# Optimization experiments

Hardware: AMD Instinct MI355X
Metric: run time of the kernel (lower is better)

The kernel has to match this reference:

```python
import jax, jax.numpy as jnp
import numpy as np

FREQ = 0.3  # oscillation_freq
EPS = 1e-12


def _spectral_normalize(W, u):
    # torch spectral_norm, training mode: one power iteration with no-grad u,v,
    # then sigma = u' @ W @ v with gradient flowing through W only.
    v = W.T @ u
    v = jax.lax.stop_gradient(v / (jnp.linalg.norm(v) + EPS))
    u2 = W @ v
    u2 = jax.lax.stop_gradient(u2 / (jnp.linalg.norm(u2) + EPS))
    sigma = u2 @ (W @ v)
    return W / sigma


def setup_inputs() -> dict:
    key = jax.random.key(0)
    ks = jax.random.split(key, 11)
    B, D_IN, H, D_OUT = 4096, 1024, 1024, 256

    def xavier(k, shape, gain=0.4):
        a = gain * np.sqrt(6.0 / (shape[0] + shape[1]))
        return jax.random.uniform(k, shape, minval=-a, maxval=a, dtype=jnp.float32)

    def bias(k, fan_in, n):
        b = 1.0 / np.sqrt(fan_in)
        return jax.random.uniform(k, (n,), minval=-b, maxval=b, dtype=jnp.float32)

    def unit(k, n):
        u = jax.random.normal(k, (n,), dtype=jnp.float32)
        return u / (jnp.linalg.norm(u) + EPS)

    return {
        "x": jax.random.normal(ks[0], (B, D_IN), dtype=jnp.float32),
        "W_in": xavier(ks[1], (H, D_IN)),
        "b_in": bias(ks[2], D_IN, H),
        "W_rec": xavier(ks[3], (H, H)),
        "b_rec": bias(ks[4], H, H),
        "W_out": xavier(ks[5], (D_OUT, H)),
        "b_out": bias(ks[6], H, D_OUT),
        "u_in": unit(ks[7], H),
        "u_rec": unit(ks[8], H),
        "u_out": unit(ks[9], D_OUT),
        "steps": 30,
    }


def reference(x, W_in, b_in, W_rec, b_rec, W_out, b_out, u_in, u_rec, u_out, steps):
    Wi = _spectral_normalize(W_in, u_in)
    Wr = _spectral_normalize(W_rec, u_rec)
    Wo = _spectral_normalize(W_out, u_out)

    x_proj = x @ Wi.T + b_in  # [B, H]
    h0 = jnp.zeros_like(x_proj)

    def step(h, t):
        modulation = 1.0 + 0.1 * jnp.sin(FREQ * t)
        h = jnp.tanh(x_proj + (h @ Wr.T + b_rec) * modulation)
        return h, None

    h, _ = jax.lax.scan(step, h0, jnp.arange(steps, dtype=jnp.float32))
    return h @ Wo.T + b_out
```

## Files before the change

kernel.cpp:

```cpp
#include <hip/hip_runtime.h>
#include <hip/hip_bf16.h>
#include <math.h>
#include <stdint.h>


#define EPSF 1e-12f

typedef short bf16x8 __attribute__((ext_vector_type(8)));
typedef float f32x4 __attribute__((ext_vector_type(4)));

struct Mods { float m[32]; };

__device__ __forceinline__ unsigned short f2bf(float f) {
  union { float f; unsigned u; } v; v.f = f;
  unsigned r = v.u + 0x7FFFu + ((v.u >> 16) & 1u);
  return (unsigned short)(r >> 16);
}

__device__ __forceinline__ unsigned cvt_pk_bf16(float lo, float hi) {
  unsigned r;
  asm("v_cvt_pk_bf16_f32 %0, %1, %2" : "=v"(r) : "v"(lo), "v"(hi));
  return r;
}

__device__ __forceinline__ float tanh_fast(float x) {
  float e = __expf(2.0f * x);
  float r = __builtin_amdgcn_rcpf(e + 1.0f);
  return fmaf(-2.0f, r, 1.0f);
}

__device__ __forceinline__ float block_reduce_sum(float x) {
#pragma unroll
  for (int o = 32; o > 0; o >>= 1) x += __shfl_down(x, o, 64);
  __shared__ float sm[8];
  int lane = threadIdx.x & 63, w = threadIdx.x >> 6;
  if (lane == 0) sm[w] = x;
  __syncthreads();
  float t = 0.f;
  if (threadIdx.x == 0) {
    int nw = (int)(blockDim.x >> 6);
    for (int i = 0; i < nw; ++i) t += sm[i];
  }
  return t;
}


__global__ void spec_col3(const float* __restrict__ Wi, const float* __restrict__ Wr,
                          const float* __restrict__ Wo, const float* __restrict__ ui,
                          const float* __restrict__ ur, const float* __restrict__ uo,
                          float* __restrict__ v) {
  int z = blockIdx.z;
  const float* W = (z == 0) ? Wi : (z == 1) ? Wr : Wo;
  const float* u = (z == 0) ? ui : (z == 1) ? ur : uo;
  int M = (z == 2) ? 256 : 1024;
  int i0 = blockIdx.y * 64;
  if (i0 >= M) return;
  int j = blockIdx.x * blockDim.x + threadIdx.x;
  float acc = 0.f;
  for (int i = i0; i < i0 + 64; ++i)
    acc += W[(size_t)i * 1024 + j] * u[i];
  atomicAdd(&v[z * 1024 + j], acc);
}

__global__ void reduce3(const float* __restrict__ Wi, const float* __restrict__ Wr,
                        const float* __restrict__ Wo, const float* __restrict__ v,
                        float* __restrict__ S) {
  int bid = blockIdx.x;
  if (bid >= 2304) {
    int z = bid - 2304;
    float acc = 0.f;
    for (int i = threadIdx.x; i < 1024; i += blockDim.x) {
      float x = v[z * 1024 + i];
      acc += x * x;
    }
    float t = block_reduce_sum(acc);
    if (threadIdx.x == 0) S[z] = t;
    return;
  }
  int z = (bid < 1024) ? 0 : (bid < 2048) ? 1 : 2;
  int row = bid - ((z == 0) ? 0 : (z == 1) ? 1024 : 2048);
  const float* W = (z == 0) ? Wi : (z == 1) ? Wr : Wo;
  const float* vv = v + z * 1024;
  float acc = 0.f;
  for (int j = threadIdx.x; j < 1024; j += blockDim.x)
    acc += W[(size_t)row * 1024 + j] * vv[j];
  float r = block_reduce_sum(acc);
  if (threadIdx.x == 0) atomicAdd(&S[3 + z], r * r);
}

__device__ __forceinline__ ushort4 cvt4e(float4 w, float s) {
  ushort4 r;
  r.x = f2bf(w.x * s); r.y = f2bf(w.y * s); r.z = f2bf(w.z * s); r.w = f2bf(w.w * s);
  return r;
}

__device__ __forceinline__ float inv_sigma(float nvsq, float wv2) {
  float nv = sqrtf(nvsq);
  float inv = 1.f / (nv + EPSF);
  float u2sq = wv2 * inv * inv;
  float nu = sqrtf(u2sq);
  float sigma = u2sq / (nu + EPSF);
  return 1.f / sigma;
}

__global__ void cvt_all(const float4* __restrict__ Wi, const float4* __restrict__ Wr,
                        const float4* __restrict__ Wo, const float4* __restrict__ x,
                        const float* __restrict__ S,
                        ushort4* __restrict__ oWi, ushort4* __restrict__ oWr,
                        ushort4* __restrict__ oWo, ushort4* __restrict__ ox) {
  float s6 = inv_sigma(S[0], S[3]);
  float s7 = inv_sigma(S[1], S[4]);
  float s8 = inv_sigma(S[2], S[5]);
  int stride = gridDim.x * blockDim.x;
  int t0 = blockIdx.x * blockDim.x + threadIdx.x;
  for (int i = t0; i < 262144; i += stride) {
    int n = i >> 8, ku = i & 255;
    int kc = ku >> 3, quad = (ku >> 1) & 3, j4 = ku & 1;
    oWi[(((n >> 4) * 32 + kc) * 64 + (n & 15) + 16 * quad) * 2 + j4] = cvt4e(Wi[i], s6);
  }
  for (int i = t0; i < 262144; i += stride) {
    int n = i >> 8, ku = i & 255;
    int kc = ku >> 3, quad = (ku >> 1) & 3, j4 = ku & 1;
    oWr[(((n >> 4) * 32 + kc) * 64 + (n & 15) + 16 * quad) * 2 + j4] = cvt4e(Wr[i], s7);
  }
  for (int i = t0; i < 65536; i += stride) {
    int n = i >> 8, ku = i & 255;
    int kc = ku >> 3, quad = (ku >> 1) & 3, j4 = ku & 1;
    oWo[(((n >> 4) * 32 + kc) * 64 + (n & 15) + 16 * quad) * 2 + j4] = cvt4e(Wo[i], s8);
  }
  for (int i = t0; i < 1048576; i += stride) {
    int m = i >> 8, ku = i & 255;
    int kc = ku >> 3, quad = (ku >> 1) & 3, j4 = ku & 1;
    ox[(size_t)(m >> 5) * 8192 +
       ((((m >> 4) & 1) * 32 + kc) * 64 + (m & 15) + 16 * quad) * 2 + j4] =
        cvt4e(x[i], 1.0f);
  }
}


template <int NF>
__device__ __forceinline__ void sweepT(const unsigned short* hsrc,
                                       const unsigned short* __restrict__ Wsrc,
                                       int lx, f32x4 acc[2][NF]) {
  bf16x8 hf[4][2], wf[4][NF];
#define LOADSET(S, KC)                                                      \
  {                                                                         \
    int kq = (KC) & 31;                                                     \
    hf[S][0] = *(const bf16x8*)(hsrc + kq * 512 + lx);                      \
    hf[S][1] = *(const bf16x8*)(hsrc + (32 + kq) * 512 + lx);               \
    _Pragma("unroll")                                                       \
    for (int nf = 0; nf < NF; ++nf)                                         \
      wf[S][nf] = *(const bf16x8*)(Wsrc + (nf * 32 + kq) * 512 + lx);       \
  }
  LOADSET(0, 0) LOADSET(1, 1) LOADSET(2, 2) LOADSET(3, 3)
#pragma unroll 1
  for (int kc = 0; kc < 32; kc += 4) {
#define STEP(S)                                                             \
    {                                                                       \
      __builtin_amdgcn_s_setprio(1);                                        \
      _Pragma("unroll")                                                     \
      for (int nf = 0; nf < NF; ++nf) {                                     \
        acc[0][nf] = __builtin_amdgcn_mfma_f32_16x16x32_bf16(               \
            wf[S][nf], hf[S][0], acc[0][nf], 0, 0, 0);                      \
        acc[1][nf] = __builtin_amdgcn_mfma_f32_16x16x32_bf16(               \
            wf[S][nf], hf[S][1], acc[1][nf], 0, 0, 0);                      \
      }                                                                     \
      __builtin_amdgcn_s_setprio(0);                                        \
      LOADSET(S, kc + S + 4)                                                \
    }
    STEP(0) STEP(1) STEP(2) STEP(3)
#undef STEP
  }
#undef LOADSET
}

__global__ __launch_bounds__(512, 1) void rnn_all(
    const unsigned short* __restrict__ xT,
    const unsigned short* __restrict__ WiT,
    const unsigned short* __restrict__ WrT,
    const unsigned short* __restrict__ WoT,
    const float* __restrict__ b_in,
    const float* __restrict__ b_rec,
    const float* __restrict__ b_out,
    float* __restrict__ outF,
    Mods mods) {
  __shared__ __align__(16) unsigned short hb[2 * 32768];

  const int tid = threadIdx.x;
  const int w = tid >> 6, lane = tid & 63;
  const int lrow = lane & 15, quad = lane >> 4;
  const int lx = lane * 8;
  const int m0 = (int)blockIdx.x * 32;
  const unsigned short* xb = xT + (size_t)blockIdx.x * 32768;

  f32x4 xpr[2][2][4];
#pragma unroll
  for (int nh = 0; nh < 2; ++nh) {
    f32x4 xa[2][4] = {};
    sweepT<4>(xb, WiT + (size_t)((w * 8 + nh * 4) * 32) * 512, lx, xa);
#pragma unroll
    for (int nf = 0; nf < 4; ++nf) {
      float4 bin4 = *(const float4*)&b_in[w * 128 + nh * 64 + nf * 16 + quad * 4];
#pragma unroll
      for (int mf = 0; mf < 2; ++mf) {
        xpr[nh][mf][nf][0] = xa[mf][nf][0] + bin4.x;
        xpr[nh][mf][nf][1] = xa[mf][nf][1] + bin4.y;
        xpr[nh][mf][nf][2] = xa[mf][nf][2] + bin4.z;
        xpr[nh][mf][nf][3] = xa[mf][nf][3] + bin4.w;
      }
    }
  }

  unsigned short* hcur = hb;
  unsigned short* hnxt = hb + 32768;
#pragma unroll 1
  for (int t = 0; t < 30; ++t) {
    const float mod = mods.m[t];
#pragma unroll
    for (int nh = 0; nh < 2; ++nh) {
      f32x4 acc[2][4] = {};
      if (t) sweepT<4>(hcur, WrT + (size_t)((w * 8 + nh * 4) * 32) * 512, lx, acc);
#pragma unroll
      for (int nf = 0; nf < 4; ++nf) {
        float4 br4 = *(const float4*)&b_rec[w * 128 + nh * 64 + nf * 16 + quad * 4];
        const int kcp = w * 4 + nh * 2 + (nf >> 1);
        const int lanep = lrow + 16 * ((nf * 2 + (quad >> 1)) & 3);
#pragma unroll
        for (int mf = 0; mf < 2; ++mf) {
          float h0 = tanh_fast(fmaf(acc[mf][nf][0] + br4.x, mod, xpr[nh][mf][nf][0]));
          float h1 = tanh_fast(fmaf(acc[mf][nf][1] + br4.y, mod, xpr[nh][mf][nf][1]));
          float h2 = tanh_fast(fmaf(acc[mf][nf][2] + br4.z, mod, xpr[nh][mf][nf][2]));
          float h3 = tanh_fast(fmaf(acc[mf][nf][3] + br4.w, mod, xpr[nh][mf][nf][3]));
          uint2 pk = {cvt_pk_bf16(h0, h1), cvt_pk_bf16(h2, h3)};
          *(uint2*)(hnxt + (mf * 32 + kcp) * 512 + lanep * 8 + (quad & 1) * 4) = pk;
        }
      }
    }
    __syncthreads();
    unsigned short* tmp = hcur; hcur = hnxt; hnxt = tmp;
  }

  {
    f32x4 ao[2][2] = {};
    sweepT<2>(hcur, WoT + (size_t)((w * 2) * 32) * 512, lx, ao);
#pragma unroll
    for (int nf = 0; nf < 2; ++nf) {
      float4 bo4 = *(const float4*)&b_out[w * 32 + nf * 16 + quad * 4];
#pragma unroll
      for (int mf = 0; mf < 2; ++mf) {
        float4 o;
        o.x = ao[mf][nf][0] + bo4.x;
        o.y = ao[mf][nf][1] + bo4.y;
        o.z = ao[mf][nf][2] + bo4.z;
        o.w = ao[mf][nf][3] + bo4.w;
        *(float4*)&outF[(size_t)(m0 + mf * 16 + lrow) * 256 + w * 32 + nf * 16 + quad * 4] = o;
      }
    }
  }
}

extern "C" void kernel_launch(void* const* d_in, const int* in_sizes, int n_in,
                              void* d_out, int out_size, void* d_ws, size_t ws_size,
                              hipStream_t stream) {
  const float* x     = (const float*)d_in[0];
  const float* W_in  = (const float*)d_in[1];
  const float* b_in  = (const float*)d_in[2];
  const float* W_rec = (const float*)d_in[3];
  const float* b_rec = (const float*)d_in[4];
  const float* W_out = (const float*)d_in[5];
  const float* b_out = (const float*)d_in[6];
  const float* u_in  = (const float*)d_in[7];
  const float* u_rec = (const float*)d_in[8];
  const float* u_out = (const float*)d_in[9];

  const int B = 4096, H = 1024;

  char* w = (char*)d_ws;
  float* S = (float*)w;
  float* v = S + 256;
  unsigned short* WiT = (unsigned short*)(w + 16384);
  unsigned short* WrT = WiT + (size_t)H * H;
  unsigned short* WoT = WrT + (size_t)H * H;
  unsigned short* xT  = WoT + (size_t)256 * H;

  hipMemsetAsync(w, 0, 16384, stream);

  dim3 t256(256);
  spec_col3<<<dim3(4, 16, 3), t256, 0, stream>>>(W_in, W_rec, W_out, u_in, u_rec, u_out, v);
  reduce3<<<2307, t256, 0, stream>>>(W_in, W_rec, W_out, v, S);
  cvt_all<<<1024, t256, 0, stream>>>((const float4*)W_in, (const float4*)W_rec,
                                     (const float4*)W_out, (const float4*)x, S,
                                     (ushort4*)WiT, (ushort4*)WrT,
                                     (ushort4*)WoT, (ushort4*)xT);

  Mods mods;
  for (int t = 0; t < 32; ++t) mods.m[t] = (float)(1.0 + 0.1 * sin(0.3 * (double)t));

  rnn_all<<<dim3(B / 32), dim3(512), 0, stream>>>(
      xT, WiT, WrT, WoT, b_in, b_rec, b_out, (float*)d_out, mods);
}
```

Baseline: 680.3 us.

## Split each batch tile across two cooperating blocks with global-memory flag sync

Each 32-row batch tile is now handled by two blocks, each owning half the hidden units. The 128-block grid becomes a 256-block cooperative launch, which uses more CUs on the GPU. The hidden state moves from LDS to a double-buffered global image, and partner blocks exchange a step counter through atomic flags. When both blocks sit on the same XCC, the acquire is replaced by a lighter cache invalidate. This adds a per-step cross-block spin wait and global-memory traffic for h, and relies on correct cache-coherence handling for correctness.

```diff
diff --git a/kernel.cpp b/kernel.cpp
--- a/kernel.cpp
+++ b/kernel.cpp
@@ -174,7 +174,7 @@
 #undef LOADSET
 }
 
-__global__ __launch_bounds__(512, 1) void rnn_all(
+__global__ __launch_bounds__(512, 2) void rnn_all(
     const unsigned short* __restrict__ xT,
     const unsigned short* __restrict__ WiT,
     const unsigned short* __restrict__ WrT,
@@ -182,79 +182,128 @@
     const float* __restrict__ b_in,
     const float* __restrict__ b_rec,
     const float* __restrict__ b_out,
+    unsigned short* __restrict__ himg,
+    unsigned* __restrict__ flags,
+    unsigned* __restrict__ xcds,
     float* __restrict__ outF,
     Mods mods) {
-  __shared__ __align__(16) unsigned short hb[2 * 32768];
-
   const int tid = threadIdx.x;
   const int w = tid >> 6, lane = tid & 63;
   const int lrow = lane & 15, quad = lane >> 4;
   const int lx = lane * 8;
-  const int m0 = (int)blockIdx.x * 32;
-  const unsigned short* xb = xT + (size_t)blockIdx.x * 32768;
-
-  f32x4 xpr[2][2][4];
-#pragma unroll
-  for (int nh = 0; nh < 2; ++nh) {
+  const int bid = (int)blockIdx.x;
+  const int p = bid & 127, s = bid >> 7;
+  const int m0 = p * 32;
+  const int nfbase = s * 32 + w * 4;
+  unsigned short* img0 = himg + (size_t)p * 65536;
+  unsigned short* img1 = img0 + 32768;
+  unsigned* myflag = flags + (size_t)(p * 2 + s) * 16;
+  unsigned* ptflag = flags + (size_t)(p * 2 + (1 - s)) * 16;
+  const unsigned short* xb = xT + (size_t)p * 32768;
+
+  unsigned myxcc = 0;
+  if (tid == 0) {
+    asm volatile("s_getreg_b32 %0, hwreg(HW_REG_XCC_ID)" : "=s"(myxcc));
+    __hip_atomic_store(xcds + (p * 2 + s), myxcc, __ATOMIC_RELEASE,
+                       __HIP_MEMORY_SCOPE_AGENT);
+  }
+
+  float4 brec4[4];
+#pragma unroll
+  for (int nf = 0; nf < 4; ++nf)
+    brec4[nf] = *(const float4*)&b_rec[s * 512 + w * 64 + nf * 16 + quad * 4];
+
+  f32x4 xpr[2][4];
+  {
     f32x4 xa[2][4] = {};
-    sweepT<4>(xb, WiT + (size_t)((w * 8 + nh * 4) * 32) * 512, lx, xa);
+    sweepT<4>(xb, WiT + (size_t)nfbase * 32 * 512, lx, xa);
 #pragma unroll
     for (int nf = 0; nf < 4; ++nf) {
-      float4 bin4 = *(const float4*)&b_in[w * 128 + nh * 64 + nf * 16 + quad * 4];
+      float4 bin4 = *(const float4*)&b_in[s * 512 + w * 64 + nf * 16 + quad * 4];
 #pragma unroll
       for (int mf = 0; mf < 2; ++mf) {
-        xpr[nh][mf][nf][0] = xa[mf][nf][0] + bin4.x;
-        xpr[nh][mf][nf][1] = xa[mf][nf][1] + bin4.y;
-        xpr[nh][mf][nf][2] = xa[mf][nf][2] + bin4.z;
-        xpr[nh][mf][nf][3] = xa[mf][nf][3] + bin4.w;
+        xpr[mf][nf][0] = xa[mf][nf][0] + bin4.x;
+        xpr[mf][nf][1] = xa[mf][nf][1] + bin4.y;
+        xpr[mf][nf][2] = xa[mf][nf][2] + bin4.z;
+        xpr[mf][nf][3] = xa[mf][nf][3] + bin4.w;
       }
     }
   }
 
-  unsigned short* hcur = hb;
-  unsigned short* hnxt = hb + 32768;
+  int fastv = 1;
+
 #pragma unroll 1
   for (int t = 0; t < 30; ++t) {
-    const float mod = mods.m[t];
-#pragma unroll
-    for (int nh = 0; nh < 2; ++nh) {
-      f32x4 acc[2][4] = {};
-      if (t) sweepT<4>(hcur, WrT + (size_t)((w * 8 + nh * 4) * 32) * 512, lx, acc);
-#pragma unroll
-      for (int nf = 0; nf < 4; ++nf) {
-        float4 br4 = *(const float4*)&b_rec[w * 128 + nh * 64 + nf * 16 + quad * 4];
-        const int kcp = w * 4 + nh * 2 + (nf >> 1);
-        const int lanep = lrow + 16 * ((nf * 2 + (quad >> 1)) & 3);
-#pragma unroll
-        for (int mf = 0; mf < 2; ++mf) {
-          float h0 = tanh_fast(fmaf(acc[mf][nf][0] + br4.x, mod, xpr[nh][mf][nf][0]));
-          float h1 = tanh_fast(fmaf(acc[mf][nf][1] + br4.y, mod, xpr[nh][mf][nf][1]));
-          float h2 = tanh_fast(fmaf(acc[mf][nf][2] + br4.z, mod, xpr[nh][mf][nf][2]));
-          float h3 = tanh_fast(fmaf(acc[mf][nf][3] + br4.w, mod, xpr[nh][mf][nf][3]));
-          uint2 pk = {cvt_pk_bf16(h0, h1), cvt_pk_bf16(h2, h3)};
-          *(uint2*)(hnxt + (mf * 32 + kcp) * 512 + lanep * 8 + (quad & 1) * 4) = pk;
+    f32x4 acc[2][4] = {};
+    if (t) {
+      if (tid == 0) {
+        while (__hip_atomic_load(ptflag, __ATOMIC_RELAXED,
+                                 __HIP_MEMORY_SCOPE_AGENT) < (unsigned)t)
+          __builtin_amdgcn_s_sleep(2);
+        if (t == 1) {
+          unsigned px = __hip_atomic_load(xcds + (p * 2 + (1 - s)),
+                                          __ATOMIC_RELAXED, __HIP_MEMORY_SCOPE_AGENT);
+          fastv = ((px & 15u) == (myxcc & 15u)) ? 1 : 0;
+        }
+        if (fastv) {
+          asm volatile("buffer_inv sc0" ::: "memory");
+        } else {
+          (void)__hip_atomic_load(ptflag, __ATOMIC_ACQUIRE, __HIP_MEMORY_SCOPE_AGENT);
         }
       }
+      __syncthreads();
+      sweepT<4>((t & 1) ? img0 : img1, WrT + (size_t)nfbase * 32 * 512, lx, acc);
+    }
+    const float mod = mods.m[t];
+    unsigned short* dst = (t & 1) ? img1 : img0;
+#pragma unroll
+    for (int nf = 0; nf < 4; ++nf) {
+      const int kcp = s * 16 + w * 2 + (nf >> 1);
+      const int lanep = lrow + 16 * (((nf & 1) * 2 + (quad >> 1)));
+#pragma unroll
+      for (int mf = 0; mf < 2; ++mf) {
+        float h0 = tanh_fast(fmaf(acc[mf][nf][0] + brec4[nf].x, mod, xpr[mf][nf][0]));
+        float h1 = tanh_fast(fmaf(acc[mf][nf][1] + brec4[nf].y, mod, xpr[mf][nf][1]));
+        float h2 = tanh_fast(fmaf(acc[mf][nf][2] + brec4[nf].z, mod, xpr[mf][nf][2]));
+        float h3 = tanh_fast(fmaf(acc[mf][nf][3] + brec4[nf].w, mod, xpr[mf][nf][3]));
+        uint2 pk = {cvt_pk_bf16(h0, h1), cvt_pk_bf16(h2, h3)};
+        *(uint2*)(dst + (mf * 32 + kcp) * 512 + lanep * 8 + (quad & 1) * 4) = pk;
+      }
     }
     __syncthreads();
-    unsigned short* tmp = hcur; hcur = hnxt; hnxt = tmp;
-  }
-
+    if (tid == 0) {
+      if (t == 0 || !fastv)
+        __hip_atomic_store(myflag, (unsigned)(t + 1), __ATOMIC_RELEASE,
+                           __HIP_MEMORY_SCOPE_AGENT);
+      else
+        __hip_atomic_store(myflag, (unsigned)(t + 1), __ATOMIC_RELAXED,
+                           __HIP_MEMORY_SCOPE_AGENT);
+    }
+  }
+
+  if (tid == 0) {
+    while (__hip_atomic_load(ptflag, __ATOMIC_RELAXED,
+                             __HIP_MEMORY_SCOPE_AGENT) < 30u)
+      __builtin_amdgcn_s_sleep(2);
+    if (fastv) {
+      asm volatile("buffer_inv sc0" ::: "memory");
+    } else {
+      (void)__hip_atomic_load(ptflag, __ATOMIC_ACQUIRE, __HIP_MEMORY_SCOPE_AGENT);
+    }
+  }
+  __syncthreads();
   {
-    f32x4 ao[2][2] = {};
-    sweepT<2>(hcur, WoT + (size_t)((w * 2) * 32) * 512, lx, ao);
-#pragma unroll
-    for (int nf = 0; nf < 2; ++nf) {
-      float4 bo4 = *(const float4*)&b_out[w * 32 + nf * 16 + quad * 4];
-#pragma unroll
-      for (int mf = 0; mf < 2; ++mf) {
-        float4 o;
-        o.x = ao[mf][nf][0] + bo4.x;
-        o.y = ao[mf][nf][1] + bo4.y;
-        o.z = ao[mf][nf][2] + bo4.z;
-        o.w = ao[mf][nf][3] + bo4.w;
-        *(float4*)&outF[(size_t)(m0 + mf * 16 + lrow) * 256 + w * 32 + nf * 16 + quad * 4] = o;
-      }
+    f32x4 ao[2][1] = {};
+    sweepT<1>(img1, WoT + (size_t)((s * 8 + w) * 32) * 512, lx, ao);
+    float4 bo4 = *(const float4*)&b_out[s * 128 + w * 16 + quad * 4];
+#pragma unroll
+    for (int mf = 0; mf < 2; ++mf) {
+      float4 o;
+      o.x = ao[mf][0][0] + bo4.x;
+      o.y = ao[mf][0][1] + bo4.y;
+      o.z = ao[mf][0][2] + bo4.z;
+      o.w = ao[mf][0][3] + bo4.w;
+      *(float4*)&outF[(size_t)(m0 + mf * 16 + lrow) * 256 + s * 128 + w * 16 + quad * 4] = o;
     }
   }
 }
@@ -282,8 +331,12 @@
   unsigned short* WrT = WiT + (size_t)H * H;
   unsigned short* WoT = WrT + (size_t)H * H;
   unsigned short* xT  = WoT + (size_t)256 * H;
+  unsigned short* himg = xT + (size_t)B * H;
+  unsigned* flags = (unsigned*)(himg + (size_t)128 * 2 * 32768);
+  unsigned* xcds  = flags + 256 * 16;
 
   hipMemsetAsync(w, 0, 16384, stream);
+  hipMemsetAsync(flags, 0, 256 * 64 + 1024, stream);
 
   dim3 t256(256);
   spec_col3<<<dim3(4, 16, 3), t256, 0, stream>>>(W_in, W_rec, W_out, u_in, u_rec, u_out, v);
@@ -295,7 +348,12 @@
 
   Mods mods;
   for (int t = 0; t < 32; ++t) mods.m[t] = (float)(1.0 + 0.1 * sin(0.3 * (double)t));
-
-  rnn_all<<<dim3(B / 32), dim3(512), 0, stream>>>(
-      xT, WiT, WrT, WoT, b_in, b_rec, b_out, (float*)d_out, mods);
-}
+  {
+    void* args[] = {(void*)&xT, (void*)&WiT, (void*)&WrT, (void*)&WoT,
+                    (void*)&b_in, (void*)&b_rec, (void*)&b_out,
+                    (void*)&himg, (void*)&flags, (void*)&xcds,
+                    (void*)&d_out, (void*)&mods};
+    hipLaunchCooperativeKernel((const void*)rnn_all, dim3(256), dim3(512),
+                               args, 0, stream);
+  }
+}
```

Result: faster. 603.3 us (-11.3%).
